# Kernel tuning notes

Hardware: AMD Instinct MI355X
Metric: run time of the kernel (lower is better)

The kernel has to match this reference:

```python
import jax, jax.numpy as jnp
import numpy as np

B = 256
N_VERTS = 10475
N_JOINTS = 55  # 1 root + 21 body + jaw + 2 eyes + 2*15 hands
NUM_BETAS = 10
NUM_EXPR = 10
POSE_BASIS = (N_JOINTS - 1) * 9  # 486
# SMPL-X kinematic tree (parent index per joint, root = -1)
PARENTS = np.array([-1,0,0,0,1,2,3,4,5,6,7,8,9,9,9,12,13,14,16,17,18,19,15,15,15,
                    20,25,26,20,28,29,20,31,32,20,34,35,20,37,38,
                    21,40,41,21,43,44,21,46,47,21,49,50,21,52,53], dtype=np.int64)


def _rodrigues(aa):
    # axis-angle [..., 3] -> rotation matrix [..., 3, 3]
    angle = jnp.linalg.norm(aa, axis=-1, keepdims=True) + 1e-8
    axis = aa / angle
    x, y, z = axis[..., 0], axis[..., 1], axis[..., 2]
    zero = jnp.zeros_like(x)
    K = jnp.stack([zero, -z, y, z, zero, -x, -y, x, zero], axis=-1).reshape(aa.shape[:-1] + (3, 3))
    s = jnp.sin(angle)[..., None]
    c = jnp.cos(angle)[..., None]
    I = jnp.eye(3, dtype=aa.dtype)
    return I + s * K + (1.0 - c) * (K @ K)


def setup_inputs() -> dict:
    key = jax.random.key(0)
    ks = jax.random.split(key, 16)
    def rots(k, nj, scale=0.2):
        aa = jax.random.normal(k, (B, nj, 3), dtype=jnp.float32) * scale
        return _rodrigues(aa)
    inp = {
        'world_rot': rots(ks[0], 1, 0.5),
        'world_tsl': jax.random.normal(ks[1], (B, 3), dtype=jnp.float32),
        'body_shape': jax.random.normal(ks[2], (B, NUM_BETAS), dtype=jnp.float32),
        'body_pose': rots(ks[3], 21),
        'left_hand_pose': rots(ks[4], 15),
        'right_hand_pose': rots(ks[5], 15),
        'expr_shape': jax.random.normal(ks[6], (B, NUM_EXPR), dtype=jnp.float32),
        'jaw_pose': rots(ks[7], 1),
        'leye_pose': rots(ks[8], 1),
        'reye_pose': rots(ks[9], 1),
        # model buffers (synthetic, SMPL-X-sized)
        'v_template': jax.random.normal(ks[10], (N_VERTS, 3), dtype=jnp.float32) * 0.3,
        'shapedirs': jax.random.normal(ks[11], (N_VERTS, 3, NUM_BETAS), dtype=jnp.float32) * 0.01,
        'expr_dirs': jax.random.normal(ks[12], (N_VERTS, 3, NUM_EXPR), dtype=jnp.float32) * 0.01,
        'posedirs': jax.random.normal(ks[13], (POSE_BASIS, N_VERTS * 3), dtype=jnp.float32) * 0.01,
        'J_regressor': jax.nn.softmax(jax.random.normal(ks[14], (N_JOINTS, N_VERTS), dtype=jnp.float32) * 4.0, axis=-1),
        'lbs_weights': jax.nn.softmax(jax.random.normal(ks[15], (N_VERTS, N_JOINTS), dtype=jnp.float32) * 4.0, axis=-1),
    }
    return inp


def _lbs(world_rot, world_tsl, body_shape, body_pose, left_hand_pose, right_hand_pose,
         expr_shape, jaw_pose, leye_pose, reye_pose,
         v_template, shapedirs, expr_dirs, posedirs, J_regressor, lbs_weights):
    dtype = v_template.dtype
    # full pose: [B, 55, 3, 3]
    full_pose = jnp.concatenate([world_rot, body_pose, jaw_pose, leye_pose, reye_pose,
                                 left_hand_pose, right_hand_pose], axis=1)
    b = full_pose.shape[0]
    # shape + expression blendshapes
    v_shaped = v_template[None] + jnp.einsum('bk,nck->bnc', body_shape, shapedirs) \
               + jnp.einsum('bk,nck->bnc', expr_shape, expr_dirs)
    # rest-pose joints [B, J, 3]
    joints = jnp.einsum('jn,bnc->bjc', J_regressor, v_shaped)
    # pose blendshapes
    ident = jnp.eye(3, dtype=dtype)
    pose_feature = (full_pose[:, 1:] - ident).reshape(b, POSE_BASIS)
    v_posed = v_shaped + (pose_feature @ posedirs).reshape(b, N_VERTS, 3)
    # relative joint locations w.r.t. parent
    rel_joints = joints.at[:, 1:].add(-joints[:, PARENTS[1:]])
    # local 4x4 transforms [B, J, 4, 4]
    top = jnp.concatenate([full_pose, rel_joints[..., None]], axis=-1)  # [B,J,3,4]
    bottom = jnp.broadcast_to(jnp.array([0., 0., 0., 1.], dtype=dtype), (b, N_JOINTS, 1, 4))
    T = jnp.concatenate([top, bottom], axis=2)
    # kinematic chain recurrence (small fixed joint count -> unrolled)
    chain = [T[:, 0]]
    for i in range(1, N_JOINTS):
        chain.append(chain[PARENTS[i]] @ T[:, i])
    A = jnp.stack(chain, axis=1)  # [B, J, 4, 4]
    posed_joints = A[..., :3, 3]
    # remove rest-pose joint offset so A maps rest -> posed
    t_corr = posed_joints - jnp.einsum('bjkl,bjl->bjk', A[..., :3, :3], joints)
    A_rel = A.at[..., :3, 3].set(t_corr)
    # linear blend skinning: per-vertex transform [B, N, 4, 4]
    T_vert = jnp.einsum('nj,bjkl->bnkl', lbs_weights, A_rel)
    verts = jnp.einsum('bnkl,bnl->bnk', T_vert[..., :3, :3], v_posed) + T_vert[..., :3, 3]
    verts = verts + world_tsl[:, None]
    joints_out = posed_joints + world_tsl[:, None]
    return verts, joints_out


def reference(world_rot, world_tsl, body_shape, body_pose, left_hand_pose, right_hand_pose,
              expr_shape, jaw_pose, leye_pose, reye_pose,
              v_template, shapedirs, expr_dirs, posedirs, J_regressor, lbs_weights):
    return _lbs(world_rot, world_tsl, body_shape, body_pose, left_hand_pose, right_hand_pose,
                expr_shape, jaw_pose, leye_pose, reye_pose,
                v_template, shapedirs, expr_dirs, posedirs, J_regressor, lbs_weights)
```

## Files before the change

kernel.cpp:

```cpp
#include <hip/hip_runtime.h>
#include <stdint.h>

#define BATCH 256
#define NV 10475
#define NVP 10496
#define NJ 55
#define PB 486
#define KS 506
#define VC (NV*3)
#define KP 512
#define BKC 32
#define NCHUNK 16
#define BN 64
#define JCH 8
#define JCHUNK 1312

typedef short bf16x8 __attribute__((ext_vector_type(8)));
typedef float f32x4  __attribute__((ext_vector_type(4)));

__constant__ int c_parents[NJ] = {
  -1,0,0,0,1,2,3,4,5,6,7,8,9,9,9,12,13,14,16,17,18,19,15,15,15,
  20,25,26,20,28,29,20,31,32,20,34,35,20,37,38,21,40,41,21,43,44,
  21,46,47,21,49,50,21,52,53};

__constant__ int c_depth[NJ] = {
  0,1,1,1,2,2,2,3,3,3,4,4,4,4,4,5,5,5,6,6,7,7,6,6,6,
  8,9,10,8,9,10,8,9,10,8,9,10,8,9,10,
  8,9,10,8,9,10,8,9,10,8,9,10,8,9,10};

__device__ __forceinline__ unsigned short f2bf(float x){
  uint32_t u = __float_as_uint(x);
  uint32_t r = (u + 0x7fffu + ((u >> 16) & 1u)) >> 16;
  return (unsigned short)r;
}
__device__ __forceinline__ float bf2f(unsigned short h){
  return __uint_as_float(((uint32_t)h) << 16);
}

__global__ __launch_bounds__(256) void k_prep(
    const float* __restrict__ lw, const float* __restrict__ sd,
    const float* __restrict__ ed, unsigned short* __restrict__ lwb,
    float* __restrict__ sdedT) {
  int bid = blockIdx.x;
  const int LWB_BLOCKS = (NVP*64)/256;
  if (bid < LWB_BLOCKS) {
    int idx = bid*256 + threadIdx.x;
    int n = idx >> 6, j = idx & 63;
    float v = (n < NV && j < NJ) ? lw[(size_t)n*NJ + j] : 0.f;
    unsigned short hi = f2bf(v);
    float lo = v - bf2f(hi);
    lwb[idx] = hi;
    lwb[(size_t)NVP*64 + idx] = f2bf(lo);
  } else {
    int idx = (bid - LWB_BLOCKS)*256 + threadIdx.x;
    if (idx >= 20*VC) return;
    int r = idx / VC, col = idx - r*VC;
    int n = col/3, c = col - n*3;
    float v = (r < 10) ? sd[(size_t)n*30 + c*10 + r]
                       : ed[(size_t)n*30 + c*10 + (r-10)];
    sdedT[idx] = v;
  }
}

__device__ __forceinline__ const float* pose_src(int j, int b,
    const float* wrot, const float* bpose, const float* jaw, const float* leye,
    const float* reye, const float* lhand, const float* rhand) {
  if (j==0)  return wrot  + b*9;
  if (j<=21) return bpose + (b*21 + (j-1))*9;
  if (j==22) return jaw   + b*9;
  if (j==23) return leye  + b*9;
  if (j==24) return reye  + b*9;
  if (j<=39) return lhand + (b*15 + (j-25))*9;
  return rhand + (b*15 + (j-40))*9;
}

__global__ __launch_bounds__(512) void k_posefeat(
    const float* __restrict__ bpose, const float* __restrict__ jaw,
    const float* __restrict__ leye, const float* __restrict__ reye,
    const float* __restrict__ lhand, const float* __restrict__ rhand,
    const float* __restrict__ bs, const float* __restrict__ es,
    unsigned short* __restrict__ pfb) {
  int b = blockIdx.x, t = threadIdx.x;
  unsigned short o = 0;
  if (t < PB){
    int jj = t/9, rc = t - jj*9;
    const float* rs = pose_src(jj+1, b, nullptr, bpose, jaw, leye, reye, lhand, rhand);
    float v = rs[rc];
    if (rc==0 || rc==4 || rc==8) v -= 1.0f;
    o = f2bf(v);
  } else if (t < 496){
    o = f2bf(bs[b*10 + (t-486)]);
  } else if (t < KS){
    o = f2bf(es[b*10 + (t-496)]);
  }
  pfb[(size_t)b*KP + t] = o;
}

__global__ __launch_bounds__(256) void k_jsmall(
    const float* __restrict__ jreg, const float* __restrict__ sd,
    const float* __restrict__ ed, const float* __restrict__ vt,
    float* __restrict__ part) {
  int ch = blockIdx.x, j = blockIdx.y;
  int t = threadIdx.x;
  float acc[63];
  #pragma unroll
  for (int s=0;s<63;s++) acc[s]=0.f;
  int n0 = ch*JCHUNK, nend = min(n0+JCHUNK, NV);
  for (int n = n0 + t; n < nend; n += 256){
    float w = jreg[(size_t)j*NV + n];
    const float* sp = sd + (size_t)n*30;
    const float* ep = ed + (size_t)n*30;
    const float* vp = vt + (size_t)n*3;
    #pragma unroll
    for (int c=0;c<3;c++){
      #pragma unroll
      for (int q=0;q<10;q++){
        acc[c*21+q]    += w*sp[c*10+q];
        acc[c*21+10+q] += w*ep[c*10+q];
      }
      acc[c*21+20] += w*vp[c];
    }
  }
  #pragma unroll
  for (int s=0;s<63;s++){
    float a = acc[s];
    #pragma unroll
    for (int d=32; d>=1; d>>=1) a += __shfl_xor(a,d);
    acc[s]=a;
  }
  __shared__ float red[4][63];
  int w = t>>6, l = t&63;
  if (l==0){
    #pragma unroll
    for (int s=0;s<63;s++) red[w][s]=acc[s];
  }
  __syncthreads();
  if (t < 63){
    float a = red[0][t]+red[1][t]+red[2][t]+red[3][t];
    part[((size_t)j*JCH+ch)*63 + t] = a;
  }
}

__global__ __launch_bounds__(192) void k_joints2(
    const float* __restrict__ part, const float* __restrict__ bs,
    const float* __restrict__ es, float* __restrict__ joints) {
  int b = blockIdx.x, t = threadIdx.x;
  if (t >= NJ*3) return;
  int j = t/3, c = t - j*3;
  float S[21];
  #pragma unroll
  for (int q=0;q<21;q++) S[q]=0.f;
  for (int ch=0; ch<JCH; ch++){
    const float* p = part + ((size_t)j*JCH+ch)*63 + c*21;
    #pragma unroll
    for (int q=0;q<21;q++) S[q] += p[q];
  }
  float a = S[20];
  #pragma unroll
  for (int q=0;q<10;q++) a += S[q]*bs[b*10+q] + S[10+q]*es[b*10+q];
  joints[(size_t)b*NJ*3 + t] = a;
}

__global__ __launch_bounds__(256) void k_chain(
    const float* __restrict__ wrot, const float* __restrict__ bpose,
    const float* __restrict__ jaw, const float* __restrict__ leye,
    const float* __restrict__ reye, const float* __restrict__ lhand,
    const float* __restrict__ rhand, const float* __restrict__ wtsl,
    const float* __restrict__ joints,
    unsigned short* __restrict__ arelb, float* __restrict__ jout) {
  const int w = threadIdx.x >> 6, lane = threadIdx.x & 63;
  const int b = blockIdx.x*4 + w;
  const int j = lane;
  const bool act = (j < NJ);

  float R[9] = {1.f,0.f,0.f, 0.f,1.f,0.f, 0.f,0.f,1.f};
  if (act){
    const float* rs = pose_src(j, b, wrot, bpose, jaw, leye, reye, lhand, rhand);
    #pragma unroll
    for (int i=0;i<9;i++) R[i]=rs[i];
  }
  float jx=0.f, jy=0.f, jz=0.f;
  if (act){
    const float* jb = joints + (size_t)b*NJ*3 + j*3;
    jx=jb[0]; jy=jb[1]; jz=jb[2];
  }
  int par = act ? c_parents[j] : 0;
  if (par < 0) par = 0;
  float px = __shfl(jx, par), py = __shfl(jy, par), pz = __shfl(jz, par);
  float t0, t1, t2;
  if (j == 0){ t0=jx; t1=jy; t2=jz; }
  else       { t0=jx-px; t1=jy-py; t2=jz-pz; }

  float M[12];
  #pragma unroll
  for (int r=0;r<3;r++){
    M[r*4+0]=R[r*3+0]; M[r*4+1]=R[r*3+1]; M[r*4+2]=R[r*3+2]; M[r*4+3]= (r==0?t0:(r==1?t1:t2));
  }
  int dep = act ? c_depth[j] : 99;

  #pragma unroll
  for (int L=1; L<=10; L++){
    float pm[12];
    #pragma unroll
    for (int i=0;i<12;i++) pm[i] = __shfl(M[i], par);
    if (dep == L){
      #pragma unroll
      for (int r=0;r<3;r++){
        float p0=pm[r*4+0], p1=pm[r*4+1], p2=pm[r*4+2], p3=pm[r*4+3];
        M[r*4+0] = p0*R[0]+p1*R[3]+p2*R[6];
        M[r*4+1] = p0*R[1]+p1*R[4]+p2*R[7];
        M[r*4+2] = p0*R[2]+p1*R[5]+p2*R[8];
        M[r*4+3] = p0*t0 + p1*t1 + p2*t2 + p3;
      }
    }
  }

  float wx=wtsl[b*3+0], wy=wtsl[b*3+1], wz=wtsl[b*3+2];
  if (act){
    jout[((size_t)b*NJ+j)*3+0] = M[3]  + wx;
    jout[((size_t)b*NJ+j)*3+1] = M[7]  + wy;
    jout[((size_t)b*NJ+j)*3+2] = M[11] + wz;
  }
  float A[12];
  #pragma unroll
  for (int r=0;r<3;r++){
    A[r*4+0]=M[r*4+0]; A[r*4+1]=M[r*4+1]; A[r*4+2]=M[r*4+2];
    A[r*4+3]=M[r*4+3] - (M[r*4+0]*jx + M[r*4+1]*jy + M[r*4+2]*jz);
  }
  unsigned short* ah = arelb + (size_t)(b*2+0)*16*64;
  unsigned short* al = arelb + (size_t)(b*2+1)*16*64;
  #pragma unroll
  for (int e=0;e<16;e++){
    float v = (e < 12 && act) ? A[e] : 0.f;
    unsigned short hi = f2bf(v);
    float lo = v - bf2f(hi);
    ah[e*64 + j] = hi;
    al[e*64 + j] = f2bf(lo);
  }
}

__global__ __launch_bounds__(256, 2) void k_vposed(
    const float* __restrict__ pd, const float* __restrict__ sdedT,
    const float* __restrict__ vt, const unsigned short* __restrict__ pfb,
    float* __restrict__ vsh) {
  const int tid  = threadIdx.x;
  const int w    = tid >> 6, lane = tid & 63;
  const int m16  = lane & 15, quad = lane >> 4;
  const int col0 = blockIdx.x * BN;

  f32x4 acc[4][4];
  #pragma unroll
  for (int i=0;i<4;i++)
    #pragma unroll
    for (int j=0;j<4;j++) acc[i][j] = (f32x4){0.f,0.f,0.f,0.f};

  int bcol[4];
  #pragma unroll
  for (int ni=0;ni<4;ni++) bcol[ni] = min(col0 + ni*16 + m16, VC-1);

  const unsigned short* pfa = pfb + (size_t)(w*64 + m16)*KP + quad*8;

  #pragma unroll 2
  for (int c=0; c<15; c++){
    const int k0 = c*BKC;
    bf16x8 a[4];
    #pragma unroll
    for (int mi=0;mi<4;mi++)
      a[mi] = *((const bf16x8*)(pfa + (size_t)mi*16*KP + k0));
    union { bf16x8 v; unsigned short s[8]; } bb[4];
    #pragma unroll
    for (int ni=0;ni<4;ni++){
      #pragma unroll
      for (int j=0;j<8;j++){
        int kk = k0 + quad*8 + j;
        bb[ni].s[j] = f2bf(pd[(size_t)kk*VC + bcol[ni]]);
      }
    }
    #pragma unroll
    for (int mi=0;mi<4;mi++)
      #pragma unroll
      for (int ni=0;ni<4;ni++)
        acc[mi][ni] = __builtin_amdgcn_mfma_f32_16x16x32_bf16(
                          a[mi], bb[ni].v, acc[mi][ni], 0, 0, 0);
  }
  {
    const int k0 = 15*BKC;
    bf16x8 a[4];
    #pragma unroll
    for (int mi=0;mi<4;mi++)
      a[mi] = *((const bf16x8*)(pfa + (size_t)mi*16*KP + k0));
    union { bf16x8 v; unsigned short s[8]; } bb[4];
    #pragma unroll
    for (int ni=0;ni<4;ni++){
      #pragma unroll
      for (int j=0;j<8;j++){
        int kk = k0 + quad*8 + j;
        float f = 0.f;
        if (kk < PB)      f = pd[(size_t)kk*VC + bcol[ni]];
        else if (kk < KS) f = sdedT[(size_t)(kk-PB)*VC + bcol[ni]];
        bb[ni].s[j] = f2bf(f);
      }
    }
    #pragma unroll
    for (int mi=0;mi<4;mi++)
      #pragma unroll
      for (int ni=0;ni<4;ni++)
        acc[mi][ni] = __builtin_amdgcn_mfma_f32_16x16x32_bf16(
                          a[mi], bb[ni].v, acc[mi][ni], 0, 0, 0);
  }
  #pragma unroll
  for (int mi=0;mi<4;mi++){
    int rbase = w*64 + mi*16 + quad*4;
    #pragma unroll
    for (int ni=0;ni<4;ni++){
      int col = col0 + ni*16 + m16;
      if (col < VC){
        float vtc = vt[col];
        #pragma unroll
        for (int r=0;r<4;r++)
          vsh[(size_t)(rbase + r)*VC + col] = acc[mi][ni][r] + vtc;
      }
    }
  }
}

__global__ __launch_bounds__(256) void k_verts(
    const unsigned short* __restrict__ lwb, const unsigned short* __restrict__ arelb,
    const float* __restrict__ wtsl, float* __restrict__ out) {
  __shared__ float sT[16*64*17];
  const int tid = threadIdx.x, w = tid >> 6, lane = tid & 63;
  const int m16 = lane & 15, quad = lane >> 4;
  const int n0 = blockIdx.x*64;
  const int b0 = blockIdx.y*16;

  bf16x8 ahh[4][2], all[4][2];
  #pragma unroll
  for (int t4=0;t4<4;t4++){
    int row = n0 + t4*16 + m16;
    #pragma unroll
    for (int kc=0;kc<2;kc++){
      ahh[t4][kc] = *((const bf16x8*)(lwb + (size_t)row*64 + kc*32 + quad*8));
      all[t4][kc] = *((const bf16x8*)(lwb + (size_t)NVP*64 + (size_t)row*64 + kc*32 + quad*8));
    }
  }
  for (int bi=0; bi<4; bi++){
    int b = b0 + w*4 + bi;
    bf16x8 bh[2], bl[2];
    #pragma unroll
    for (int kc=0;kc<2;kc++){
      bh[kc] = *((const bf16x8*)(arelb + ((size_t)(b*2+0)*16 + m16)*64 + kc*32 + quad*8));
      bl[kc] = *((const bf16x8*)(arelb + ((size_t)(b*2+1)*16 + m16)*64 + kc*32 + quad*8));
    }
    f32x4 acc[4];
    #pragma unroll
    for (int t4=0;t4<4;t4++) acc[t4] = (f32x4){0.f,0.f,0.f,0.f};
    #pragma unroll
    for (int t4=0;t4<4;t4++)
      #pragma unroll
      for (int kc=0;kc<2;kc++){
        acc[t4] = __builtin_amdgcn_mfma_f32_16x16x32_bf16(ahh[t4][kc], bh[kc], acc[t4], 0,0,0);
        acc[t4] = __builtin_amdgcn_mfma_f32_16x16x32_bf16(all[t4][kc], bh[kc], acc[t4], 0,0,0);
        acc[t4] = __builtin_amdgcn_mfma_f32_16x16x32_bf16(ahh[t4][kc], bl[kc], acc[t4], 0,0,0);
      }
    if (m16 < 12){
      int slot = w*4 + bi;
      #pragma unroll
      for (int t4=0;t4<4;t4++){
        #pragma unroll
        for (int r=0;r<4;r++){
          int vert = t4*16 + quad*4 + r;
          sT[(slot*64 + vert)*17 + m16] = acc[t4][r];
        }
      }
    }
  }
  __syncthreads();
  #pragma unroll
  for (int it=0; it<4; it++){
    int pid = it*256 + tid;
    int bb = pid >> 6, v = pid & 63;
    int n = n0 + v;
    if (n >= NV) continue;
    int b = b0 + bb;
    const float* Tp = &sT[(bb*64 + v)*17];
    float T[12];
    #pragma unroll
    for (int e=0;e<12;e++) T[e] = Tp[e];
    float* op = out + ((size_t)b*NV + n)*3;
    float x=op[0], y=op[1], z=op[2];
    float tx=wtsl[b*3+0], ty=wtsl[b*3+1], tz=wtsl[b*3+2];
    op[0] = T[0]*x + T[1]*y + T[2] *z + T[3]  + tx;
    op[1] = T[4]*x + T[5]*y + T[6] *z + T[7]  + ty;
    op[2] = T[8]*x + T[9]*y + T[10]*z + T[11] + tz;
  }
}

extern "C" void kernel_launch(void* const* d_in, const int* in_sizes, int n_in,
                              void* d_out, int out_size, void* d_ws, size_t ws_size,
                              hipStream_t stream) {
  const float* wrot   = (const float*)d_in[0];
  const float* wtsl   = (const float*)d_in[1];
  const float* bshape = (const float*)d_in[2];
  const float* bpose  = (const float*)d_in[3];
  const float* lhand  = (const float*)d_in[4];
  const float* rhand  = (const float*)d_in[5];
  const float* eshape = (const float*)d_in[6];
  const float* jaw    = (const float*)d_in[7];
  const float* leye   = (const float*)d_in[8];
  const float* reye   = (const float*)d_in[9];
  const float* vt     = (const float*)d_in[10];
  const float* sd     = (const float*)d_in[11];
  const float* ed     = (const float*)d_in[12];
  const float* pd     = (const float*)d_in[13];
  const float* jreg   = (const float*)d_in[14];
  const float* lw     = (const float*)d_in[15];
  float* out = (float*)d_out;

  float* vsh  = out;
  float* jout = out + (size_t)BATCH*NV*3;

  float* ws     = (float*)d_ws;
  float* joints = ws;
  float* part   = joints + (size_t)BATCH*NJ*3;
  float* sdedT  = part   + (size_t)NJ*JCH*63;
  unsigned short* pfb   = (unsigned short*)(sdedT + (size_t)20*VC);
  unsigned short* lwb   = pfb + (size_t)BATCH*KP;
  unsigned short* arelb = lwb + (size_t)2*NVP*64;

  const int PREP_BLOCKS = (NVP*64)/256 + (20*VC + 255)/256;

  k_prep    <<<PREP_BLOCKS, 256, 0, stream>>>(lw, sd, ed, lwb, sdedT);
  k_posefeat<<<BATCH, 512, 0, stream>>>(bpose, jaw, leye, reye, lhand, rhand,
                                        bshape, eshape, pfb);
  k_jsmall  <<<dim3(JCH, NJ), 256, 0, stream>>>(jreg, sd, ed, vt, part);
  k_joints2 <<<BATCH, 192, 0, stream>>>(part, bshape, eshape, joints);
  k_chain   <<<64, 256, 0, stream>>>(wrot, bpose, jaw, leye, reye, lhand, rhand,
                                     wtsl, joints, arelb, jout);
  k_vposed  <<<(VC+BN-1)/BN, 256, 0, stream>>>(pd, sdedT, vt, pfb, vsh);
  k_verts   <<<dim3(NVP/64, 16), 256, 0, stream>>>(lwb, arelb, wtsl, out);
}
```

Before: 255.4 us.

## Swap MFMA operand roles in k_verts to apply transforms in registers

The per-vertex skinning kernel now puts the joint transforms as the A operand and the vertex weights as the B operand. Each lane then holds one full row of the 3x4 transform for its vertex directly in the accumulator. This removes the shared-memory staging buffer and the block-wide barrier, and each wave handles 16 vertices across 16 batches. In exchange, three lanes each read the same x,y,z inputs and write single scattered floats, and the arelb loads are repeated per batch inside the loop.

```diff
diff --git a/kernel.cpp b/kernel.cpp
--- a/kernel.cpp
+++ b/kernel.cpp
@@ -327,71 +327,43 @@
 __global__ __launch_bounds__(256) void k_verts(
     const unsigned short* __restrict__ lwb, const unsigned short* __restrict__ arelb,
     const float* __restrict__ wtsl, float* __restrict__ out) {
-  __shared__ float sT[16*64*17];
   const int tid = threadIdx.x, w = tid >> 6, lane = tid & 63;
   const int m16 = lane & 15, quad = lane >> 4;
-  const int n0 = blockIdx.x*64;
+  const int n = blockIdx.x*64 + w*16 + m16;
   const int b0 = blockIdx.y*16;
 
-  bf16x8 ahh[4][2], all[4][2];
-  #pragma unroll
-  for (int t4=0;t4<4;t4++){
-    int row = n0 + t4*16 + m16;
+  bf16x8 wh[2], wl[2];
+  #pragma unroll
+  for (int kc=0;kc<2;kc++){
+    wh[kc] = *((const bf16x8*)(lwb + (size_t)n*64 + kc*32 + quad*8));
+    wl[kc] = *((const bf16x8*)(lwb + (size_t)NVP*64 + (size_t)n*64 + kc*32 + quad*8));
+  }
+  const bool vok = (n < NV) && (quad < 3);
+
+  #pragma unroll 2
+  for (int bi=0; bi<16; bi++){
+    int b = b0 + bi;
+    const unsigned short* ah = arelb + (size_t)(b*2+0)*16*64;
+    const unsigned short* al = arelb + (size_t)(b*2+1)*16*64;
+    bf16x8 Ah[2], Al[2];
     #pragma unroll
     for (int kc=0;kc<2;kc++){
-      ahh[t4][kc] = *((const bf16x8*)(lwb + (size_t)row*64 + kc*32 + quad*8));
-      all[t4][kc] = *((const bf16x8*)(lwb + (size_t)NVP*64 + (size_t)row*64 + kc*32 + quad*8));
-    }
-  }
-  for (int bi=0; bi<4; bi++){
-    int b = b0 + w*4 + bi;
-    bf16x8 bh[2], bl[2];
+      Ah[kc] = *((const bf16x8*)(ah + m16*64 + kc*32 + quad*8));
+      Al[kc] = *((const bf16x8*)(al + m16*64 + kc*32 + quad*8));
+    }
+    f32x4 acc = (f32x4){0.f,0.f,0.f,0.f};
     #pragma unroll
     for (int kc=0;kc<2;kc++){
-      bh[kc] = *((const bf16x8*)(arelb + ((size_t)(b*2+0)*16 + m16)*64 + kc*32 + quad*8));
-      bl[kc] = *((const bf16x8*)(arelb + ((size_t)(b*2+1)*16 + m16)*64 + kc*32 + quad*8));
-    }
-    f32x4 acc[4];
-    #pragma unroll
-    for (int t4=0;t4<4;t4++) acc[t4] = (f32x4){0.f,0.f,0.f,0.f};
-    #pragma unroll
-    for (int t4=0;t4<4;t4++)
-      #pragma unroll
-      for (int kc=0;kc<2;kc++){
-        acc[t4] = __builtin_amdgcn_mfma_f32_16x16x32_bf16(ahh[t4][kc], bh[kc], acc[t4], 0,0,0);
-        acc[t4] = __builtin_amdgcn_mfma_f32_16x16x32_bf16(all[t4][kc], bh[kc], acc[t4], 0,0,0);
-        acc[t4] = __builtin_amdgcn_mfma_f32_16x16x32_bf16(ahh[t4][kc], bl[kc], acc[t4], 0,0,0);
-      }
-    if (m16 < 12){
-      int slot = w*4 + bi;
-      #pragma unroll
-      for (int t4=0;t4<4;t4++){
-        #pragma unroll
-        for (int r=0;r<4;r++){
-          int vert = t4*16 + quad*4 + r;
-          sT[(slot*64 + vert)*17 + m16] = acc[t4][r];
-        }
-      }
-    }
-  }
-  __syncthreads();
-  #pragma unroll
-  for (int it=0; it<4; it++){
-    int pid = it*256 + tid;
-    int bb = pid >> 6, v = pid & 63;
-    int n = n0 + v;
-    if (n >= NV) continue;
-    int b = b0 + bb;
-    const float* Tp = &sT[(bb*64 + v)*17];
-    float T[12];
-    #pragma unroll
-    for (int e=0;e<12;e++) T[e] = Tp[e];
-    float* op = out + ((size_t)b*NV + n)*3;
-    float x=op[0], y=op[1], z=op[2];
-    float tx=wtsl[b*3+0], ty=wtsl[b*3+1], tz=wtsl[b*3+2];
-    op[0] = T[0]*x + T[1]*y + T[2] *z + T[3]  + tx;
-    op[1] = T[4]*x + T[5]*y + T[6] *z + T[7]  + ty;
-    op[2] = T[8]*x + T[9]*y + T[10]*z + T[11] + tz;
+      acc = __builtin_amdgcn_mfma_f32_16x16x32_bf16(Ah[kc], wh[kc], acc, 0,0,0);
+      acc = __builtin_amdgcn_mfma_f32_16x16x32_bf16(Al[kc], wh[kc], acc, 0,0,0);
+      acc = __builtin_amdgcn_mfma_f32_16x16x32_bf16(Ah[kc], wl[kc], acc, 0,0,0);
+    }
+    if (vok){
+      float* op = out + ((size_t)b*NV + n)*3;
+      float x = op[0], y = op[1], z = op[2];
+      float o = acc[0]*x + acc[1]*y + acc[2]*z + acc[3] + wtsl[b*3+quad];
+      op[quad] = o;
+    }
   }
 }
 
```

Measured after the change: 298.7 us. 17.0% more time.
